# Kernel optimization log

Hardware: AMD Instinct MI355X
Metric: run time of the kernel (lower is better)

The kernel has to match this reference:

```python
import jax, jax.numpy as jnp
import numpy as np

EPS = 1e-5

def layer_norm(x, gamma, beta):
    m = x.mean(axis=-1, keepdims=True)
    v = ((x - m) ** 2).mean(axis=-1, keepdims=True)  # correction=0
    return (x - m) / jnp.sqrt(v + EPS) * gamma + beta

def setup_inputs() -> dict:
    key = jax.random.key(0)
    B, T, E, H = 2, 2048, 1024, 16
    hd = E // H
    dff = 4 * E
    ks = jax.random.split(key, 10)
    s = 0.02
    return {
        "x": jax.random.normal(ks[0], (B, T, E), jnp.float32),
        "wq": jax.random.normal(ks[1], (H, E, hd), jnp.float32) * s,
        "wk": jax.random.normal(ks[2], (H, E, hd), jnp.float32) * s,
        "wv": jax.random.normal(ks[3], (H, E, hd), jnp.float32) * s,
        "w_proj": jax.random.normal(ks[4], (E, E), jnp.float32) * s,
        "b_proj": jnp.zeros((E,), jnp.float32),
        "gamma1": jnp.ones((E,), jnp.float32),
        "beta1": jnp.zeros((E,), jnp.float32),
        "gamma2": jnp.ones((E,), jnp.float32),
        "beta2": jnp.zeros((E,), jnp.float32),
        "w1": jax.random.normal(ks[5], (E, dff), jnp.float32) * s,
        "b1": jnp.zeros((dff,), jnp.float32),
        "w2": jax.random.normal(ks[6], (dff, E), jnp.float32) * s,
        "b2": jnp.zeros((E,), jnp.float32),
    }

def reference(x, wq, wk, wv, w_proj, b_proj, gamma1, beta1, gamma2, beta2, w1, b1, w2, b2):
    B, T, E = x.shape
    H, _, hd = wq.shape
    # pre-attention norm; NOTE: residual uses the normalized value (as in source)
    h = layer_norm(x, gamma1, beta1)
    # per-head projections, vectorized over heads: [B,H,T,hd]
    q = jnp.einsum('bte,hek->bhtk', h, wq)
    k = jnp.einsum('bte,hek->bhtk', h, wk)
    v = jnp.einsum('bte,hek->bhtk', h, wv)
    att = jnp.einsum('bhtk,bhsk->bhts', q, k) / jnp.sqrt(jnp.float32(hd))
    causal = jnp.tril(jnp.ones((T, T), bool))
    att = jnp.where(causal, att, -jnp.inf)
    p = jax.nn.softmax(att, axis=-1)  # dropout is identity in eval
    o = jnp.einsum('bhts,bhsk->bhtk', p, v)
    o = o.transpose(0, 2, 1, 3).reshape(B, T, E)  # concat heads
    attn_out = o @ w_proj + b_proj
    x2 = h + attn_out
    # pre-FFN norm; residual again uses normalized value
    h2 = layer_norm(x2, gamma2, beta2)
    ffn = jax.nn.relu(h2 @ w1 + b1) @ w2 + b2
    return h2 + ffn
```

## Files before the change

kernel.cpp:

```cpp
#include <hip/hip_runtime.h>
#include <stdint.h>

typedef unsigned short u16;
typedef __attribute__((ext_vector_type(8))) short short8;
typedef __attribute__((ext_vector_type(4))) short short4_t;
typedef __attribute__((ext_vector_type(4))) float f32x4;

__device__ __forceinline__ float b2f(u16 u){ union{unsigned i; float f;}v; v.i=((unsigned)u)<<16; return v.f; }
__device__ __forceinline__ u16 f2b(float f){ unsigned x=__float_as_uint(f); return (u16)((x + 0x7fffu + ((x>>16)&1u))>>16); }

#if __has_builtin(__builtin_amdgcn_exp2f)
#define EXP2F(x) __builtin_amdgcn_exp2f(x)
#else
#define EXP2F(x) exp2f(x)
#endif

#if __has_builtin(__builtin_amdgcn_mfma_f32_16x16x16_bf16)
#define MFMA16(a,b,c) __builtin_amdgcn_mfma_f32_16x16x16_bf16(a,b,c,0,0,0)
#elif __has_builtin(__builtin_amdgcn_mfma_f32_16x16x16bf16_1k)
#define MFMA16(a,b,c) __builtin_amdgcn_mfma_f32_16x16x16bf16_1k(a,b,c,0,0,0)
#else
static __device__ __forceinline__ f32x4 mfma16_asm(short4_t a, short4_t b, f32x4 c){
  __asm__("v_mfma_f32_16x16x16_bf16 %0, %1, %2, %3" : "=v"(c) : "v"(a), "v"(b), "0"(c));
  return c;
}
#define MFMA16(a,b,c) mfma16_asm(a,b,c)
#endif

__device__ __forceinline__ void async16(const void* g, void* l){
  __builtin_amdgcn_global_load_lds((const __attribute__((address_space(1))) void*)g,
                                   (__attribute__((address_space(3))) void*)l, 16, 0, 0);
}

__device__ __forceinline__ short4_t pack4(f32x4 s){
  unsigned u0 = (__float_as_uint(s[0]) + 0x8000u) >> 16;
  unsigned u1 = (__float_as_uint(s[1]) + 0x8000u) & 0xffff0000u;
  unsigned u2 = (__float_as_uint(s[2]) + 0x8000u) >> 16;
  unsigned u3 = (__float_as_uint(s[3]) + 0x8000u) & 0xffff0000u;
  union { unsigned v[2]; short4_t s4; } r;
  r.v[0] = u0 | u1; r.v[1] = u2 | u3;
  return r.s4;
}

template<int IN_F32>
__global__ __launch_bounds__(256) void ln_kernel(const void* __restrict__ xin,
    const float* __restrict__ g, const float* __restrict__ b, u16* __restrict__ y)
{
  const int E = 1024;
  int row = blockIdx.x, t = threadIdx.x;
  float f0,f1,f2,f3;
  if (IN_F32){
    const float* xr = (const float*)xin + (size_t)row*E;
    float4 xv = *(const float4*)(xr + t*4);
    f0=xv.x; f1=xv.y; f2=xv.z; f3=xv.w;
  } else {
    const u16* xr = (const u16*)xin + (size_t)row*E;
    ushort4 xv = *(const ushort4*)(xr + t*4);
    f0=b2f(xv.x); f1=b2f(xv.y); f2=b2f(xv.z); f3=b2f(xv.w);
  }
  float s1 = f0+f1+f2+f3;
  float s2 = f0*f0+f1*f1+f2*f2+f3*f3;
  #pragma unroll
  for (int off=32; off>=1; off>>=1){ s1 += __shfl_xor(s1,off); s2 += __shfl_xor(s2,off); }
  __shared__ float red[8];
  int w = t>>6;
  if ((t&63)==0){ red[w]=s1; red[4+w]=s2; }
  __syncthreads();
  float S1 = red[0]+red[1]+red[2]+red[3];
  float S2 = red[4]+red[5]+red[6]+red[7];
  float mean = S1*(1.0f/E);
  float var  = S2*(1.0f/E) - mean*mean;
  float inv  = rsqrtf(var + 1e-5f);
  float4 gv = *(const float4*)(g + t*4);
  float4 bv = *(const float4*)(b + t*4);
  ushort4 o;
  o.x = f2b((f0-mean)*inv*gv.x+bv.x);
  o.y = f2b((f1-mean)*inv*gv.y+bv.y);
  o.z = f2b((f2-mean)*inv*gv.z+bv.z);
  o.w = f2b((f3-mean)*inv*gv.w+bv.w);
  *(ushort4*)(y + (size_t)row*E + t*4) = o;
}

__global__ __launch_bounds__(256) void transpose_bt(const float* __restrict__ src, u16* __restrict__ dst,
                                                    int ld_src, int ld_dst)
{
  __shared__ u16 tile[64*66];
  int c0 = blockIdx.x*64, r0 = blockIdx.y*64;
  int t = threadIdx.x;
  #pragma unroll
  for (int i=0;i<16;++i){
    int lin = i*256 + t;
    int rr = lin>>6, cc = lin&63;
    tile[cc*66+rr] = f2b(src[(size_t)(r0+rr)*ld_src + c0+cc]);
  }
  __syncthreads();
  #pragma unroll
  for (int i=0;i<16;++i){
    int lin = i*256 + t;
    int cc = lin>>6, rr = lin&63;
    dst[(size_t)(c0+cc)*ld_dst + r0+rr] = tile[cc*66+rr];
  }
}

__global__ __launch_bounds__(256) void qkv_repack(const float* __restrict__ wq, const float* __restrict__ wk,
                                                  const float* __restrict__ wv, u16* __restrict__ dst)
{
  __shared__ u16 tile[64*66];
  int e0 = blockIdx.x*64;
  int sel = blockIdx.y>>4, h = blockIdx.y&15;
  const float* src = (sel==0?wq:(sel==1?wk:wv)) + (size_t)h*1024*64;
  int t = threadIdx.x;
  #pragma unroll
  for (int i=0;i<16;++i){
    int lin=i*256+t; int rr=lin>>6, cc=lin&63;
    tile[cc*66+rr] = f2b(src[(size_t)(e0+rr)*64 + cc]);
  }
  __syncthreads();
  #pragma unroll
  for (int i=0;i<16;++i){
    int lin=i*256+t; int cc=lin>>6, rr=lin&63;
    dst[(size_t)(sel*1024 + h*64 + cc)*1024 + e0+rr] = tile[cc*66+rr];
  }
}

__global__ __launch_bounds__(256) void vtrans(const u16* __restrict__ qkv, u16* __restrict__ VT)
{
  __shared__ u16 tile[64*66];
  int bh = blockIdx.y, bb = bh>>4, h = bh&15;
  int s0 = blockIdx.x*64;
  const u16* src = qkv + ((size_t)(bb*2048) + s0)*3072 + 2048 + h*64;
  int t = threadIdx.x;
  int sr = t>>3, c0 = (t&7)*8;
  #pragma unroll
  for (int half=0; half<2; ++half){
    const u16* p = src + (size_t)(sr+half*32)*3072 + c0;
    ushort4 v0 = *(const ushort4*)p;
    ushort4 v1 = *(const ushort4*)(p+4);
    uint* d = (uint*)(tile + (sr+half*32)*66 + c0);
    d[0] = (uint)v0.x | ((uint)v0.y<<16);
    d[1] = (uint)v0.z | ((uint)v0.w<<16);
    d[2] = (uint)v1.x | ((uint)v1.y<<16);
    d[3] = (uint)v1.z | ((uint)v1.w<<16);
  }
  __syncthreads();
  u16* out = VT + (size_t)bh*64*2048 + s0;
  int dw = t>>3, sc = (t&7)*8;
  #pragma unroll
  for (int half=0; half<2; ++half){
    int d = dw + half*32;
    short8 pk;
    #pragma unroll
    for (int j=0;j<8;++j) pk[j] = (short)tile[(sc+j)*66 + d];
    *(short8*)(out + (size_t)d*2048 + sc) = pk;
  }
}

template<int MI>
__global__ __launch_bounds__(256, 3) void gemm_bt(const u16* __restrict__ A, const u16* __restrict__ Bt,
    u16* __restrict__ C, float* __restrict__ Cf, int M, int N, int K,
    const float* __restrict__ bias, const u16* __restrict__ residual, int do_relu, int gx)
{
  __shared__ __align__(16) u16 As[2][MI*32*64];
  __shared__ __align__(16) u16 Bs[2][128*64];
  int t = threadIdx.x;
  int bid = blockIdx.y * gridDim.x + blockIdx.x;
  int xcd = bid & 7, slot = bid >> 3;
  int gy = 8 / gx;
  int rx = gridDim.x / gx, ry = gridDim.y / gy;
  int col_b = (xcd % gx) * rx + (slot % rx);
  int row_b = (xcd / gx) * ry + (slot / rx);
  int row0 = row_b*(MI*32), col0 = col_b*128;
  int l = t&63, w = t>>6;
  int wm = (w>>1)*(MI*16), wn = (w&1)*64;
  int lr = l&15, lq = l>>4;
  (void)M;

  f32x4 acc[MI][4];
  #pragma unroll
  for (int i=0;i<MI;++i)
    #pragma unroll
    for (int j=0;j<4;++j) acc[i][j] = f32x4{0.f,0.f,0.f,0.f};

  const u16* gA = A  + (size_t)(row0 + (t>>3))*K + (((t&7)^((t>>3)&7))<<3);
  const u16* gB = Bt + (size_t)(col0 + (t>>3))*K + (((t&7)^((t>>3)&7))<<3);
  const size_t rnd = (size_t)32*K;
  int nk = K>>6;

  #pragma unroll
  for (int r=0;r<MI;++r) async16(gA + r*rnd, As[0] + r*2048 + t*8);
  #pragma unroll
  for (int r=0;r<4;++r)  async16(gB + r*rnd, Bs[0] + r*2048 + t*8);

  int sw8 = (lr&7);
  for (int kt=0; kt<nk; ++kt){
    int cur = kt&1;
    __syncthreads();
    if (kt+1 < nk){
      int ko = (kt+1)<<6;
      #pragma unroll
      for (int r=0;r<MI;++r) async16(gA + r*rnd + ko, As[cur^1] + r*2048 + t*8);
      #pragma unroll
      for (int r=0;r<4;++r)  async16(gB + r*rnd + ko, Bs[cur^1] + r*2048 + t*8);
    }
    const u16* as = As[cur];
    const u16* bs = Bs[cur];
    #pragma unroll
    for (int kk=0;kk<2;++kk){
      int so = (((kk*4+lq)^sw8))<<3;
      short8 a[MI], b[4];
      #pragma unroll
      for (int i=0;i<MI;++i) a[i] = *(const short8*)(as + (wm+i*16+lr)*64 + so);
      #pragma unroll
      for (int j=0;j<4;++j)  b[j] = *(const short8*)(bs + (wn+j*16+lr)*64 + so);
      #pragma unroll
      for (int i=0;i<MI;++i)
        #pragma unroll
        for (int j=0;j<4;++j)
          acc[i][j] = __builtin_amdgcn_mfma_f32_16x16x32_bf16(a[i], b[j], acc[i][j], 0,0,0);
    }
  }

  #pragma unroll
  for (int i=0;i<MI;++i){
    #pragma unroll
    for (int j=0;j<4;++j){
      int col = col0 + wn + j*16 + lr;
      float bv = bias ? bias[col] : 0.0f;
      #pragma unroll
      for (int r=0;r<4;++r){
        int row = row0 + wm + i*16 + lq*4 + r;
        float v = acc[i][j][r] + bv;
        if (do_relu) v = fmaxf(v, 0.0f);
        if (residual) v += b2f(residual[(size_t)row*N + col]);
        if (Cf) Cf[(size_t)row*N + col] = v;
        else    C [(size_t)row*N + col] = f2b(v);
      }
    }
  }
}

__global__ __launch_bounds__(256,4) void attn_kernel(const u16* __restrict__ QKV,
    const u16* __restrict__ VT, u16* __restrict__ O)
{
  const int T=2048, LD=3072, E=1024;
  int bid = blockIdx.y * gridDim.x + blockIdx.x;
  int xcd = bid & 7, slot = bid >> 3;
  int idx = slot & 31, grp = slot >> 5;
  int qt = (grp & 1) ? idx : 31 - idx;
  int bh = xcd*4 + grp;
  int bb = bh>>4, h = bh&15;
  const u16* base = QKV + (size_t)bb*T*LD;
  const u16* Qp = base + h*64;
  const u16* Kp = base + 1024 + h*64;
  const u16* Vtp = VT + (size_t)bh*64*2048;
  int t = threadIdx.x, l = t&63, w = t>>6;
  int lr = l&15, lq = l>>4;

  __shared__ __align__(16) u16 Ks[2][64*64];
  __shared__ __align__(16) u16 Vs[2][64*64];

  const float QSC = 0.125f*1.44269504f;
  int q0 = qt*64 + w*16;
  short8 aq[2];
  #pragma unroll
  for (int kk=0;kk<2;++kk){
    short8 raw = *(const short8*)(Qp + (size_t)(q0+lr)*LD + kk*32 + lq*8);
    short8 sc;
    #pragma unroll
    for (int j=0;j<8;++j) sc[j] = (short)f2b(b2f((u16)raw[j])*QSC);
    aq[kk]=sc;
  }

  float mrun = -3e38f, lrun = 0.f;
  f32x4 Oacc[4];
  #pragma unroll
  for (int dt=0;dt<4;++dt) Oacc[dt] = f32x4{0.f,0.f,0.f,0.f};

  int kc = (l&7) ^ (l>>3);
  int ra = 8*w + (l>>3);

  async16(Kp  + (size_t)ra*LD        + kc*8, Ks[0] + t*8);
  async16(Kp  + (size_t)(ra+32)*LD   + kc*8, Ks[0] + 2048 + t*8);
  async16(Vtp + (size_t)ra*2048      + kc*8, Vs[0] + t*8);
  async16(Vtp + (size_t)(ra+32)*2048 + kc*8, Vs[0] + 2048 + t*8);

  for (int it=0; it<=qt; ++it){
    int s0 = it*64, cur = it&1;
    __syncthreads();
    if (it < qt){
      int sn = s0+64;
      u16* kd = Ks[cur^1]; u16* vd = Vs[cur^1];
      async16(Kp  + (size_t)(sn+ra)*LD        + kc*8, kd + t*8);
      async16(Kp  + (size_t)(sn+ra+32)*LD     + kc*8, kd + 2048 + t*8);
      async16(Vtp + (size_t)ra*2048      + sn + kc*8, vd + t*8);
      async16(Vtp + (size_t)(ra+32)*2048 + sn + kc*8, vd + 2048 + t*8);
    }
    const u16* ks = Ks[cur];
    const u16* vs = Vs[cur];

    f32x4 S[4];
    #pragma unroll
    for (int st=0; st<4; ++st){
      short8 kf0 = *(const short8*)(ks + (st*16+lr)*64 + ((lq  )^(lr&7))*8);
      short8 kf1 = *(const short8*)(ks + (st*16+lr)*64 + ((4+lq)^(lr&7))*8);
      f32x4 z = f32x4{0.f,0.f,0.f,0.f};
      z = __builtin_amdgcn_mfma_f32_16x16x32_bf16(kf0, aq[0], z, 0,0,0);
      z = __builtin_amdgcn_mfma_f32_16x16x32_bf16(kf1, aq[1], z, 0,0,0);
      S[st] = z;
    }
    if (it == qt){
      int qg = q0 + lr;
      #pragma unroll
      for (int st=0;st<4;++st)
        #pragma unroll
        for (int r=0;r<4;++r){
          int sg = s0 + st*16 + lq*4 + r;
          if (sg > qg) S[st][r] = -3e38f;
        }
    }
    float m = S[0][0];
    #pragma unroll
    for (int st=0;st<4;++st)
      #pragma unroll
      for (int r=0;r<4;++r) m = fmaxf(m, S[st][r]);
    m = fmaxf(m, __shfl_xor(m,16));
    m = fmaxf(m, __shfl_xor(m,32));
    float mnew = fmaxf(mrun, m);
    float alpha = EXP2F(mrun - mnew);
    mrun = mnew;
    float ssum = 0.f;
    #pragma unroll
    for (int st=0;st<4;++st)
      #pragma unroll
      for (int r=0;r<4;++r){ float p = EXP2F(S[st][r]-mnew); S[st][r]=p; ssum+=p; }
    ssum += __shfl_xor(ssum,16);
    ssum += __shfl_xor(ssum,32);
    lrun = lrun*alpha + ssum;
    short4_t pk[4];
    #pragma unroll
    for (int st=0;st<4;++st) pk[st] = pack4(S[st]);
    float af[4];
    #pragma unroll
    for (int r=0;r<4;++r) af[r] = __shfl(alpha, lq*4+r);
    #pragma unroll
    for (int dt=0;dt<4;++dt)
      #pragma unroll
      for (int r=0;r<4;++r) Oacc[dt][r] *= af[r];
    #pragma unroll
    for (int st=0;st<4;++st){
      #pragma unroll
      for (int dt=0;dt<4;++dt){
        short4_t vf = *(const short4_t*)(vs + (dt*16+lr)*64 + ((2*st+(lq>>1))^(lr&7))*8 + (lq&1)*4);
        Oacc[dt] = MFMA16(pk[st], vf, Oacc[dt]);
      }
    }
  }
  float linv[4];
  #pragma unroll
  for (int r=0;r<4;++r) linv[r] = 1.0f/__shfl(lrun, lq*4+r);
  #pragma unroll
  for (int dt=0;dt<4;++dt)
    #pragma unroll
    for (int r=0;r<4;++r){
      int qg = q0 + lq*4 + r;
      O[(size_t)(bb*T+qg)*E + h*64 + dt*16 + lr] = f2b(Oacc[dt][r]*linv[r]);
    }
}

extern "C" void kernel_launch(void* const* d_in, const int* in_sizes, int n_in,
                              void* d_out, int out_size, void* d_ws, size_t ws_size,
                              hipStream_t stream)
{
  (void)in_sizes; (void)n_in; (void)out_size; (void)ws_size;
  const float* x     = (const float*)d_in[0];
  const float* wq    = (const float*)d_in[1];
  const float* wk    = (const float*)d_in[2];
  const float* wv    = (const float*)d_in[3];
  const float* wproj = (const float*)d_in[4];
  const float* bproj = (const float*)d_in[5];
  const float* g1    = (const float*)d_in[6];
  const float* be1   = (const float*)d_in[7];
  const float* g2    = (const float*)d_in[8];
  const float* be2   = (const float*)d_in[9];
  const float* w1    = (const float*)d_in[10];
  const float* b1    = (const float*)d_in[11];
  const float* w2    = (const float*)d_in[12];
  const float* b2    = (const float*)d_in[13];
  float* out = (float*)d_out;

  char* ws = (char*)d_ws;
  size_t off = 0;
  auto alloc = [&](size_t bytes)->void*{ void* p = ws + off; off += (bytes + 255) & ~(size_t)255; return p; };
  u16* hnorm  = (u16*)alloc((size_t)4096*1024*2);
  u16* qkv    = (u16*)alloc((size_t)4096*3072*2);
  u16* VT     = (u16*)alloc((size_t)32*64*2048*2);
  u16* attnO  = (u16*)alloc((size_t)4096*1024*2);
  u16* x2     = (u16*)alloc((size_t)4096*1024*2);
  u16* h2     = (u16*)alloc((size_t)4096*1024*2);
  u16* ffn1   = (u16*)alloc((size_t)4096*4096*2);
  u16* wqkvT  = (u16*)alloc((size_t)3072*1024*2);
  u16* wprojT = (u16*)alloc((size_t)1024*1024*2);
  u16* w1T    = (u16*)alloc((size_t)4096*1024*2);
  u16* w2T    = (u16*)alloc((size_t)1024*4096*2);

  qkv_repack  <<<dim3(16,48),256,0,stream>>>(wq,wk,wv,wqkvT);
  transpose_bt<<<dim3(16,16),256,0,stream>>>(wproj, wprojT, 1024, 1024);
  transpose_bt<<<dim3(64,16),256,0,stream>>>(w1,    w1T,    4096, 1024);
  transpose_bt<<<dim3(16,64),256,0,stream>>>(w2,    w2T,    1024, 4096);

  ln_kernel<1><<<4096,256,0,stream>>>(x, g1, be1, hnorm);
  gemm_bt<4><<<dim3(24,32),256,0,stream>>>(hnorm, wqkvT, qkv, nullptr, 4096,3072,1024, nullptr, nullptr, 0, 8);
  vtrans<<<dim3(32,32),256,0,stream>>>(qkv, VT);
  attn_kernel<<<dim3(32,32),256,0,stream>>>(qkv, VT, attnO);
  gemm_bt<2><<<dim3(8,64),256,0,stream>>>(attnO, wprojT, x2, nullptr, 4096,1024,1024, bproj, hnorm, 0, 2);
  ln_kernel<0><<<4096,256,0,stream>>>(x2, g2, be2, h2);
  gemm_bt<4><<<dim3(32,32),256,0,stream>>>(h2, w1T, ffn1, nullptr, 4096,4096,1024, b1, nullptr, 1, 8);
  gemm_bt<2><<<dim3(8,64),256,0,stream>>>(ffn1, w2T, nullptr, out, 4096,1024,4096, b2, h2, 0, 2);
}
```

Before: 372.9 us.

## Add 256x256-tile 512-thread GEMM for QKV and FFN1 projections

```diff
diff --git a/kernel.cpp b/kernel.cpp
--- a/kernel.cpp
+++ b/kernel.cpp
@@ -239,6 +239,173 @@
   }
 }
 
+__global__ __launch_bounds__(512,2) void gemm256(const u16* __restrict__ A, const u16* __restrict__ Bt,
+    u16* __restrict__ C, float* __restrict__ Cf, int N, int K,
+    const float* __restrict__ bias, const u16* __restrict__ residual, int do_relu, int gx)
+{
+  __shared__ __align__(16) u16 As[2][256*64];
+  __shared__ __align__(16) u16 Bs[2][256*64];
+  int t = threadIdx.x;
+  int bid = blockIdx.y*gridDim.x + blockIdx.x;
+  int xcd = bid & 7, slot = bid >> 3;
+  int gy = 8/gx;
+  int rx = gridDim.x/gx, ry = gridDim.y/gy;
+  int col_b = (xcd%gx)*rx + slot%rx;
+  int row_b = (xcd/gx)*ry + slot/rx;
+  int row0 = row_b*256, col0 = col_b*256;
+  int l = t&63, w = t>>6;
+  int wr = w>>2, wc = w&3;
+  int lr = l&15, lq = l>>4, sw = lr&7;
+
+  f32x4 acc[8][4];
+  #pragma unroll
+  for (int m=0;m<8;++m)
+    #pragma unroll
+    for (int n=0;n<4;++n) acc[m][n] = f32x4{0.f,0.f,0.f,0.f};
+
+  int i = t>>3, c8 = t&7;
+  int swc = (c8 ^ (i&7))*8;
+  const u16* aS[4]; const u16* bS[4];
+  {
+    int la[4] = { i, 128+i, 64+i, 192+i };
+    #pragma unroll
+    for (int s=0;s<4;++s){
+      aS[s] = A + (size_t)(row0 + la[s])*K + swc;
+      int p = s*64 + i;
+      int lb = ((p>>5)&3)*64 + (p>>7)*32 + (p&31);
+      bS[s] = Bt + (size_t)(col0 + lb)*K + swc;
+    }
+  }
+  int nk = K>>6;
+
+  async16(aS[0], As[0] + 0*4096 + t*8);
+  async16(aS[1], As[0] + 1*4096 + t*8);
+  async16(bS[0], Bs[0] + 0*4096 + t*8);
+  async16(bS[1], Bs[0] + 1*4096 + t*8);
+  async16(bS[2], Bs[0] + 2*4096 + t*8);
+  async16(bS[3], Bs[0] + 3*4096 + t*8);
+  async16(aS[2], As[0] + 2*4096 + t*8);
+  async16(aS[3], As[0] + 3*4096 + t*8);
+  asm volatile("s_waitcnt vmcnt(4)" ::: "memory");
+  __builtin_amdgcn_s_barrier();
+
+  short8 af[4][2], bf[2][2];
+
+#define RD_A(qm) \
+  _Pragma("unroll") \
+  for (int mm=0;mm<4;++mm){ \
+    _Pragma("unroll") \
+    for (int kk=0;kk<2;++kk) \
+      af[mm][kk] = *(const short8*)(asC + ((qm)*128 + wr*64 + mm*16 + lr)*64 + (((kk*4+lq)^sw)<<3)); \
+  }
+#define RD_B(qn) \
+  _Pragma("unroll") \
+  for (int nn=0;nn<2;++nn){ \
+    _Pragma("unroll") \
+    for (int kk=0;kk<2;++kk) \
+      bf[nn][kk] = *(const short8*)(bsC + ((qn)*128 + wc*32 + nn*16 + lr)*64 + (((kk*4+lq)^sw)<<3)); \
+  }
+#define MMQ(qm,qn) \
+  __builtin_amdgcn_s_setprio(1); \
+  _Pragma("unroll") \
+  for (int mm=0;mm<4;++mm){ \
+    _Pragma("unroll") \
+    for (int nn=0;nn<2;++nn){ \
+      _Pragma("unroll") \
+      for (int kk=0;kk<2;++kk) \
+        acc[(qm)*4+mm][(qn)*2+nn] = __builtin_amdgcn_mfma_f32_16x16x32_bf16(af[mm][kk], bf[nn][kk], acc[(qm)*4+mm][(qn)*2+nn], 0,0,0); \
+    } \
+  } \
+  __builtin_amdgcn_s_setprio(0);
+#define BARW \
+  __builtin_amdgcn_s_barrier(); \
+  asm volatile("s_waitcnt lgkmcnt(0)" ::: "memory"); \
+  __builtin_amdgcn_sched_barrier(0);
+#define PIN __builtin_amdgcn_sched_barrier(0);
+
+  for (int kt=0; kt<nk-1; ++kt){
+    int cur = kt&1;
+    const u16* asC = As[cur]; const u16* bsC = Bs[cur];
+    u16* asN = As[cur^1];    u16* bsN = Bs[cur^1];
+    int ko = (kt+1)<<6;
+    RD_A(0); RD_B(0);
+    async16(aS[0]+ko, asN + 0*4096 + t*8);
+    async16(aS[1]+ko, asN + 1*4096 + t*8);
+    PIN;
+    asm volatile("s_waitcnt vmcnt(4)" ::: "memory");
+    BARW;
+    MMQ(0,0);
+    __builtin_amdgcn_s_barrier();
+    RD_B(1);
+    async16(bS[0]+ko, bsN + 0*4096 + t*8);
+    async16(bS[1]+ko, bsN + 1*4096 + t*8);
+    PIN;
+    asm volatile("s_waitcnt vmcnt(4)" ::: "memory");
+    BARW;
+    MMQ(0,1);
+    __builtin_amdgcn_s_barrier();
+    RD_A(1);
+    async16(bS[2]+ko, bsN + 2*4096 + t*8);
+    async16(bS[3]+ko, bsN + 3*4096 + t*8);
+    PIN;
+    BARW;
+    MMQ(1,1);
+    __builtin_amdgcn_s_barrier();
+    RD_B(0);
+    async16(aS[2]+ko, asN + 2*4096 + t*8);
+    async16(aS[3]+ko, asN + 3*4096 + t*8);
+    PIN;
+    asm volatile("s_waitcnt vmcnt(4)" ::: "memory");
+    BARW;
+    MMQ(1,0);
+    __builtin_amdgcn_s_barrier();
+  }
+  {
+    int cur = (nk-1)&1;
+    const u16* asC = As[cur]; const u16* bsC = Bs[cur];
+    RD_A(0); RD_B(0);
+    asm volatile("s_waitcnt vmcnt(2)" ::: "memory");
+    BARW;
+    MMQ(0,0);
+    __builtin_amdgcn_s_barrier();
+    RD_B(1);
+    asm volatile("s_waitcnt vmcnt(0)" ::: "memory");
+    BARW;
+    MMQ(0,1);
+    __builtin_amdgcn_s_barrier();
+    RD_A(1);
+    BARW;
+    MMQ(1,1);
+    __builtin_amdgcn_s_barrier();
+    RD_B(0);
+    BARW;
+    MMQ(1,0);
+  }
+#undef RD_A
+#undef RD_B
+#undef MMQ
+#undef BARW
+#undef PIN
+
+  #pragma unroll
+  for (int m=0;m<8;++m){
+    #pragma unroll
+    for (int n=0;n<4;++n){
+      int col = col0 + wc*64 + n*16 + lr;
+      float bv = bias ? bias[col] : 0.0f;
+      #pragma unroll
+      for (int r=0;r<4;++r){
+        int row = row0 + wr*128 + m*16 + lq*4 + r;
+        float v = acc[m][n][r] + bv;
+        if (do_relu) v = fmaxf(v, 0.0f);
+        if (residual) v += b2f(residual[(size_t)row*N + col]);
+        if (Cf) Cf[(size_t)row*N + col] = v;
+        else    C [(size_t)row*N + col] = f2b(v);
+      }
+    }
+  }
+}
+
 __global__ __launch_bounds__(256,4) void attn_kernel(const u16* __restrict__ QKV,
     const u16* __restrict__ VT, u16* __restrict__ O)
 {
@@ -409,11 +576,11 @@
   transpose_bt<<<dim3(16,64),256,0,stream>>>(w2,    w2T,    1024, 4096);
 
   ln_kernel<1><<<4096,256,0,stream>>>(x, g1, be1, hnorm);
-  gemm_bt<4><<<dim3(24,32),256,0,stream>>>(hnorm, wqkvT, qkv, nullptr, 4096,3072,1024, nullptr, nullptr, 0, 8);
+  gemm256<<<dim3(12,16),512,0,stream>>>(hnorm, wqkvT, qkv, nullptr, 3072, 1024, nullptr, nullptr, 0, 4);
   vtrans<<<dim3(32,32),256,0,stream>>>(qkv, VT);
   attn_kernel<<<dim3(32,32),256,0,stream>>>(qkv, VT, attnO);
   gemm_bt<2><<<dim3(8,64),256,0,stream>>>(attnO, wprojT, x2, nullptr, 4096,1024,1024, bproj, hnorm, 0, 2);
   ln_kernel<0><<<4096,256,0,stream>>>(x2, g2, be2, h2);
-  gemm_bt<4><<<dim3(32,32),256,0,stream>>>(h2, w1T, ffn1, nullptr, 4096,4096,1024, b1, nullptr, 1, 8);
+  gemm256<<<dim3(16,16),512,0,stream>>>(h2, w1T, ffn1, nullptr, 4096, 1024, b1, nullptr, 1, 4);
   gemm_bt<2><<<dim3(8,64),256,0,stream>>>(ffn1, w2T, nullptr, out, 4096,1024,4096, b2, h2, 0, 2);
 }
```

After: 365.8 us. Within noise of the previous version (-1.9%).
